# Kernel optimization log

Hardware: AMD Instinct MI355X
Metric: run time of the kernel (lower is better)

## Reference

```python
import jax, jax.numpy as jnp
import numpy as np

B = 65536
DIM = 8
HIS_LEN = 5
KIND_LEN = 10
HIS_ITEM_DIM = (1 + KIND_LEN) * DIM  # 88
ALL_DIM = DIM * (5 + KIND_LEN) + HIS_ITEM_DIM  # 208


def _linear_params(key, in_dim, out_dim):
    k1, k2 = jax.random.split(key)
    bound = 1.0 / np.sqrt(in_dim)
    w = jax.random.uniform(k1, (out_dim, in_dim), jnp.float32, -bound, bound)
    b = jax.random.uniform(k2, (out_dim,), jnp.float32, -bound, bound)
    return w, b


def setup_inputs() -> dict:
    key = jax.random.key(0)
    ks = jax.random.split(key, 20)
    inp = {
        'userid': jax.random.randint(ks[0], (B, 1), 0, 1000000),
        'itemid': jax.random.randint(ks[1], (B, 1), 0, 1000000),
        'user_age': jax.random.randint(ks[2], (B, 1), 0, 8),
        'gender': jax.random.randint(ks[3], (B, 1), 0, 3),
        'user_occupation': jax.random.randint(ks[4], (B, 1), 0, 25),
        'item_kind': jax.random.randint(ks[5], (B, KIND_LEN), 0, 20),
        'item_id_his': jax.random.randint(ks[6], (B, HIS_LEN), 0, 1000000),
        'item_kind_his': jax.random.randint(ks[7], (B, HIS_LEN, KIND_LEN), 0, 20),
        'user_emb': jax.random.normal(ks[8], (1000000, DIM), jnp.float32),
        'item_emb': jax.random.normal(ks[9], (1000000, DIM), jnp.float32),
        'age_emb': jax.random.normal(ks[10], (8, DIM), jnp.float32),
        'gender_emb': jax.random.normal(ks[11], (3, DIM), jnp.float32),
        'occ_emb': jax.random.normal(ks[12], (25, DIM), jnp.float32),
        'kind_emb': jax.random.normal(ks[13], (20, DIM), jnp.float32),
    }
    act_dims = [(HIS_ITEM_DIM * 3, 64), (64, 32), (32, 1)]
    for i, (di, do) in enumerate(act_dims, 1):
        w, b = _linear_params(jax.random.fold_in(key, 100 + i), di, do)
        inp[f'act_w{i}'], inp[f'act_b{i}'] = w, b
    mlp_dims = [(ALL_DIM, 128), (128, 64), (64, 32), (32, 1)]
    for i, (di, do) in enumerate(mlp_dims, 1):
        w, b = _linear_params(jax.random.fold_in(key, 200 + i), di, do)
        inp[f'mlp_w{i}'], inp[f'mlp_b{i}'] = w, b
    return inp


def _forward(userid, itemid, user_age, gender, user_occupation, item_kind,
             item_id_his, item_kind_his, user_emb, item_emb, age_emb,
             gender_emb, occ_emb, kind_emb,
             act_w1, act_b1, act_w2, act_b2, act_w3, act_b3,
             mlp_w1, mlp_b1, mlp_w2, mlp_b2, mlp_w3, mlp_b3, mlp_w4, mlp_b4):
    b = userid.shape[0]
    user_w = user_emb[userid]          # [b,1,8]
    item_w = item_emb[itemid]          # [b,1,8]
    age_w = age_emb[user_age]          # [b,1,8]
    gen_w = gender_emb[gender]         # [b,1,8]
    occ_w = occ_emb[user_occupation]   # [b,1,8]
    kind_w = kind_emb[item_kind]       # [b,10,8]
    kind_w = kind_w * (item_kind != 0)[..., None].astype(kind_w.dtype)

    # history: vectorized over his_len
    his_item_w = item_emb[item_id_his]           # [b,5,8]
    his_kind_w = kind_emb[item_kind_his]         # [b,5,10,8]
    his_kind_w = his_kind_w * (item_kind_his != 0)[..., None].astype(his_kind_w.dtype)
    his_feature = jnp.concatenate([his_item_w[:, :, None, :], his_kind_w], axis=2)
    his_feature = his_feature.reshape(b, HIS_LEN, HIS_ITEM_DIM)  # [b,5,88]

    item_feat_now = jnp.concatenate([item_w, kind_w], axis=1).reshape(b, 1, HIS_ITEM_DIM)
    item_feat_now = jnp.broadcast_to(item_feat_now, (b, HIS_LEN, HIS_ITEM_DIM))

    # ActUnit: i_in = [i1, i1-i2, i2]; score = MLP(i_in); act_weight = i1 * score
    i1, i2 = his_feature, item_feat_now
    i_in = jnp.concatenate([i1, i1 - i2, i2], axis=-1)  # [b,5,264]
    h = jax.nn.relu(jnp.einsum('bsd,od->bso', i_in, act_w1) + act_b1)
    h = jax.nn.relu(jnp.einsum('bsd,od->bso', h, act_w2) + act_b2)
    score = jnp.einsum('bsd,od->bso', h, act_w3) + act_b3  # [b,5,1]
    act_weight = i1 * score
    his_pool = jnp.sum(his_feature * act_weight, axis=1)  # [b,88]

    all_feat = jnp.concatenate([user_w, item_w, age_w, gen_w, occ_w, kind_w], axis=1).reshape(b, -1)
    all_feat = jnp.concatenate([all_feat, his_pool], axis=-1)  # [b,208]

    h = jax.nn.relu(all_feat @ mlp_w1.T + mlp_b1)
    h = jax.nn.relu(h @ mlp_w2.T + mlp_b2)
    h = jax.nn.relu(h @ mlp_w3.T + mlp_b3)
    logit = h @ mlp_w4.T + mlp_b4  # [b,1]
    return jax.nn.sigmoid(logit)


def reference(userid, itemid, user_age, gender, user_occupation, item_kind,
              item_id_his, item_kind_his, user_emb, item_emb, age_emb,
              gender_emb, occ_emb, kind_emb,
              act_w1, act_b1, act_w2, act_b2, act_w3, act_b3,
              mlp_w1, mlp_b1, mlp_w2, mlp_b2, mlp_w3, mlp_b3, mlp_w4, mlp_b4):
    return _forward(userid, itemid, user_age, gender, user_occupation, item_kind,
                    item_id_his, item_kind_his, user_emb, item_emb, age_emb,
                    gender_emb, occ_emb, kind_emb,
                    act_w1, act_b1, act_w2, act_b2, act_w3, act_b3,
                    mlp_w1, mlp_b1, mlp_w2, mlp_b2, mlp_w3, mlp_b3, mlp_w4, mlp_b4)
```

## Files before the change

### kernel.cpp

```cpp
#include <hip/hip_runtime.h>
#include <cstdint>
#include <math.h>

#define BATCH    65536
#define HIS_LEN  5
#define KIND_LEN 10
#define SB       64
#define NTH      256

typedef float    v2f __attribute__((ext_vector_type(2)));
typedef float    v4f __attribute__((ext_vector_type(4)));
typedef _Float16 v2h __attribute__((ext_vector_type(2)));
typedef _Float16 v8h __attribute__((ext_vector_type(8)));
__device__ __forceinline__ v2f mk2(float a, float b){ v2f r; r.x=a; r.y=b; return r; }
#define C2H(u)  __builtin_bit_cast(v2h,(unsigned)(u))
#define C8H(u4) __builtin_bit_cast(v8h,(u4))

#if __has_builtin(__builtin_amdgcn_fdot2)
__device__ __forceinline__ float FD2(v2h a, v2h b, float c){
  return __builtin_amdgcn_fdot2(a, b, c, false);
}
#else
__device__ __forceinline__ float FD2(v2h a, v2h b, float c){
  return c + (float)a.x*(float)b.x + (float)a.y*(float)b.y;
}
#endif

__device__ __forceinline__ unsigned short f2h(float f){
  return __builtin_bit_cast(unsigned short, (_Float16)f);
}
__device__ __forceinline__ unsigned pack2h(float a, float b){
  return (unsigned)f2h(a) | ((unsigned)f2h(b) << 16);
}
__device__ __forceinline__ v2h pkh(float a, float b){
  return __builtin_bit_cast(v2h, __builtin_amdgcn_cvt_pkrtz(a, b));
}

__device__ __forceinline__ void wlf(){
  asm volatile("s_waitcnt lgkmcnt(0)" ::: "memory");
  __builtin_amdgcn_sched_barrier(0);
}

#define OFF_HW1F 0
#define OFF_AW2F 6144
#define OFF_PF   7168
#define OFF_M3H  7428
#define OFF_MW1F 8452
#define OFF_MB1  22788
#define OFF_MW2F 22916
#define PREP_N   27012
#define AW2F4 1536
#define M3H4  1857
#define MW1F4 2113
#define MW2F4 5729

#define X2B   0
#define X1B   832
#define H1B   1664
#define H2B   2240
#define M3HL  2816
#define LAB1  12312
#define LAB2  12376
#define LW3   12408
#define LAB3  12440
#define LMB2  12441
#define LMB3  12505
#define LM4   12537
#define LMB4  12569
#define MB1F  12572
#define LDSF  12700

typedef const float* fp;

__device__ __forceinline__ float m1s_val(fp m1, int o, int q, int t){
  if(t >= 52) return 0.f;
  int src;
  if(t<8){ int E = (q==0)?0:(8+8*q); src = E + t; }
  else if(t<30){ int d=t-8; int idx = 8*(d>>1)+2*q+(d&1);
                 src = (idx<8) ? (8+idx) : (32+idx); }
  else { int d=t-30; int idx = 8*(d>>1)+2*q+(d&1); src = 120+idx; }
  return m1[o*208 + src];
}
__device__ __forceinline__ float m1k(fp m1, int o, int k){
  return m1s_val(m1, o, k/56, k%56);
}
__device__ __forceinline__ float w1c_val(fp aw1, int o, int q, int h, int d){
  if(d >= 22) return 0.f;
  int idx = 8*(d>>1) + 2*q + (d&1);
  return h ? (aw1[o*264+176+idx] - aw1[o*264+88+idx])
           : (aw1[o*264+idx]     + aw1[o*264+88+idx]);
}
__device__ __forceinline__ float hw1v(fp aw1, int o, int k){
  int h = (k >= 96) ? 1 : 0;
  int kk = k - 96*h;
  int q = kk/24, d = kk%24;
  return (d<22) ? w1c_val(aw1,o,q,h,d) : 0.f;
}

__global__ void din_prep(fp aw1, fp ab1, fp aw2, fp ab2, fp aw3, fp ab3,
                         fp m1,  fp mb1, fp m2,  fp mb2, fp m3,  fp mb3,
                         fp m4,  fp mb4, float* __restrict__ ws){
  int j = blockIdx.x*blockDim.x + threadIdx.x;
  unsigned* wsu = (unsigned*)ws;
  if(j < 6144){
    int frag = j>>2, jr = j&3;
    int lane = frag & 63, nt = frag >> 6;
    int n = nt/6, t = nt%6;
    int o = 16*n + (lane&15);
    int k0 = t*32 + ((lane>>4)<<3) + 2*jr;
    wsu[OFF_HW1F + j] = pack2h(hw1v(aw1,o,k0), hw1v(aw1,o,k0+1));
    return;
  } j -= 6144;
  if(j < 1024){
    int frag = j>>2, jr = j&3;
    int lane = frag & 63, nt = frag >> 6;
    int n2 = nt>>1, t2 = nt&1;
    int o = 16*n2 + (lane&15);
    int k0 = t2*32 + ((lane>>4)<<3) + 2*jr;
    wsu[OFF_AW2F + j] = pack2h(aw2[o*64 + k0], aw2[o*64 + k0+1]);
    return;
  } j -= 1024;
  if(j < 258){
    float v;
    if(j < 64)       v = ab1[j];
    else if(j < 96)  v = ab2[j-64];
    else if(j < 128) v = aw3[j-96];
    else if(j < 129) v = ab3[0];
    else if(j < 193) v = mb2[j-129];
    else if(j < 225) v = mb3[j-193];
    else if(j < 257) v = m4[j-225];
    else             v = mb4[0];
    ws[OFF_PF + j] = v; return;
  } j -= 258;
  if(j < 2){ ws[OFF_PF+258+j] = 0.f; return; } j -= 2;
  if(j < 1024){
    int qq = j>>8, rr = j&255, ip = rr>>5, dw = rr&31;
    wsu[OFF_M3H + j] = pack2h(m3[dw*64 + 16*qq + 2*ip], m3[dw*64 + 16*qq + 2*ip+1]);
    return;
  } j -= 1024;
  if(j < 14336){
    int frag = j>>2, jr = j&3;
    int lane = frag & 63, nt = frag >> 6;
    int n = nt/7, t = nt - 7*n;
    int o = 16*n + (lane&15);
    int k0 = t*32 + ((lane>>4)<<3) + 2*jr;
    wsu[OFF_MW1F + j] = pack2h(m1k(m1,o,k0), m1k(m1,o,k0+1));
    return;
  } j -= 14336;
  if(j < 128){ ws[OFF_MB1 + j] = mb1[j]; return; } j -= 128;
  if(j < 4096){
    int frag = j>>2, jr = j&3;
    int lane = frag & 63, nt = frag >> 6;
    int n2 = nt>>2, t2 = nt&3;
    int o = 16*n2 + (lane&15);
    int k0 = t2*32 + ((lane>>4)<<3) + 2*jr;
    wsu[OFF_MW2F + j] = pack2h(m2[o*128 + k0], m2[o*128 + k0+1]);
    return;
  }
}

template<int CTL>
__device__ __forceinline__ float qp(float v){
  return __uint_as_float((unsigned)__builtin_amdgcn_update_dpp(
      0, (int)__float_as_uint(v), CTL, 0xF, 0xF, true));
}
__device__ __forceinline__ float bsum4(float v){
  v += qp<0xB1>(v);
  v += qp<0x4E>(v);
  return v;
}

__device__ __forceinline__ void ldst16(void* l, const void* g){
  __builtin_amdgcn_global_load_lds(
      (const __attribute__((address_space(1))) unsigned int*)(uintptr_t)g,
      (__attribute__((address_space(3))) unsigned int*)(uintptr_t)l, 16, 0, 0);
}
__device__ __forceinline__ void ldst4(void* l, const void* g){
  __builtin_amdgcn_global_load_lds(
      (const __attribute__((address_space(1))) unsigned int*)(uintptr_t)g,
      (__attribute__((address_space(3))) unsigned int*)(uintptr_t)l, 4, 0, 0);
}

__device__ __forceinline__ void gather_h(const float2* __restrict__ itemp,
                                         const float2* __restrict__ kindp,
                                         int item_idx, const int* __restrict__ kidx,
                                         int q, v2h* f){
  float2 v = itemp[item_idx*4 + q];
  f[0] = pkh(v.x, v.y);
  #pragma unroll
  for(int r=0;r<KIND_LEN;r++){
    int ki = kidx[r];
    float2 w = kindp[ki*4 + q];
    float mx = ki ? w.x : 0.f, my = ki ? w.y : 0.f;
    f[1+r] = pkh(mx, my);
  }
}

__device__ __forceinline__ void write_X(float4* ls4, int base, int wid, int q,
                                        const v2h* f){
  unsigned xd[12];
  #pragma unroll
  for(int r=0;r<11;r++) xd[r] = __builtin_bit_cast(unsigned, f[r]);
  xd[11] = 0;
  uint4* xp = (uint4*)(ls4 + base + wid*13 + 3*q);
  #pragma unroll
  for(int c=0;c<3;c++){
    uint4 t; t.x=xd[4*c]; t.y=xd[4*c+1]; t.z=xd[4*c+2]; t.w=xd[4*c+3];
    xp[c] = t;
  }
}

__global__ void __launch_bounds__(NTH, 3)
din_main(const int* __restrict__ userid, const int* __restrict__ itemid,
         const int* __restrict__ age,    const int* __restrict__ gen,
         const int* __restrict__ occ,    const int* __restrict__ item_kind,
         const int* __restrict__ his_id, const int* __restrict__ his_kind,
         const float2* __restrict__ user_emb, const float2* __restrict__ item_emb,
         const float2* __restrict__ age_emb,  const float2* __restrict__ gen_emb,
         const float2* __restrict__ occ_emb,  const float2* __restrict__ kind_emb,
         const float* __restrict__ ws, float* __restrict__ out){
  const int tid  = threadIdx.x;
  const int q    = tid & 3;
  const int sl   = (tid & 63) >> 2;
  const int wv   = __builtin_amdgcn_readfirstlane(tid >> 6);
  const int wid  = wv*16 + sl;
  const int b    = blockIdx.x*SB + wid;
  const int l    = tid & 63;
  const int sr   = wv*16 + (l&15);
  const int kb   = l >> 4;

  __shared__ __align__(16) float ls[LDSF];
  float4* ls4 = (float4*)ls;
  const uint4* lsu4 = (const uint4*)ls;
  const float* wsc = ws;
  const float4* ws4 = (const float4*)ws;
  const uint4* wsu4 = (const uint4*)ws;

  ldst4(ls + LAB1 + tid, wsc + OFF_PF + tid);
  if(tid < 2)   ldst4(ls + LAB1 + 256 + tid, wsc + OFF_PF + 256 + tid);
  if(tid < 128) ldst4(ls + MB1F + tid, wsc + OFF_MB1 + tid);
  ldst16(ls4 + M3HL + (tid>>6)*66 + (tid&63), ws4 + M3H4 + tid);

  {
    v2h i2t[11];
    gather_h(item_emb, kind_emb, itemid[b], item_kind + b*KIND_LEN, q, i2t);
    write_X(ls4, X2B, wid, q, i2t);
  }
  v2h i1c[11], i1n[11];
  gather_h(item_emb, kind_emb, his_id[b*HIS_LEN], his_kind + b*HIS_LEN*KIND_LEN,
           q, i1c);

  v2f poolv[11];
  #pragma unroll
  for(int d=0;d<11;d++) poolv[d]=mk2(0.f,0.f);
  v2h i2h[11];
  float2 exr[4];

  __syncthreads();

  float hb1[4], hb2[2], w3r[8];
  #pragma unroll
  for(int n=0;n<4;n++)  hb1[n] = ls[LAB1 + 16*n + (l&15)];
  #pragma unroll
  for(int n2=0;n2<2;n2++) hb2[n2] = ls[LAB2 + 16*n2 + (l&15)];
  #pragma unroll
  for(int k=0;k<8;k++)  w3r[k] = ls[LW3 + 8*q + k];
  const float ab3v = ls[LAB3];
  uint4 awf[4];
  #pragma unroll
  for(int t=0;t<4;t++) awf[t] = wsu4[AW2F4 + t*64 + l];

  #pragma unroll 1
  for(int s=0;s<5;s++){
    wlf();
    write_X(ls4, X1B, wid, q, i1c);
    if(s < 4){
      gather_h(item_emb, kind_emb, his_id[b*HIS_LEN+s+1],
               his_kind + (b*HIS_LEN+s+1)*KIND_LEN, q, i1n);
    } else {
      gather_h(item_emb, kind_emb, itemid[b], item_kind + b*KIND_LEN, q, i2h);
      const float2* ep = (q==0)? user_emb : (q==1)? age_emb : (q==2)? gen_emb : occ_emb;
      int ei = (q==0)? userid[b] : (q==1)? age[b] : (q==2)? gen[b] : occ[b];
      #pragma unroll
      for(int k=0;k<4;k++) exr[k] = ep[ei*4+k];
    }
    wlf();
    {
      uint4 a1[6];
      #pragma unroll
      for(int t=0;t<3;t++) a1[t]   = lsu4[X1B + sr*13 + 4*t + kb];
      #pragma unroll
      for(int t=0;t<3;t++) a1[3+t] = lsu4[X2B + sr*13 + 4*t + kb];
      _Float16* h1p = (_Float16*)(ls4 + H1B);
      #pragma unroll
      for(int n=0;n<4;n++){
        float bb = hb1[n];
        v4f c = {bb,bb,bb,bb};
        #pragma unroll
        for(int t=0;t<6;t++){
          uint4 bw = wsu4[(n*6+t)*64 + l];
          c = __builtin_amdgcn_mfma_f32_16x16x32_f16(C8H(a1[t]), C8H(bw), c, 0, 0, 0);
        }
        #pragma unroll
        for(int i=0;i<4;i++)
          h1p[(16*wv + 4*kb + i)*72 + 16*n + (l&15)] = (_Float16)fmaxf(c[i],0.f);
      }
    }
    wlf();
    {
      uint4 a2[2];
      #pragma unroll
      for(int t=0;t<2;t++) a2[t] = lsu4[H1B + sr*9 + 4*t + kb];
      float* h2p = (float*)(ls4 + H2B);
      #pragma unroll
      for(int n2=0;n2<2;n2++){
        float bb = hb2[n2];
        v4f c = {bb,bb,bb,bb};
        #pragma unroll
        for(int t=0;t<2;t++){
          uint4 bw = awf[n2*2+t];
          c = __builtin_amdgcn_mfma_f32_16x16x32_f16(C8H(a2[t]), C8H(bw), c, 0, 0, 0);
        }
        #pragma unroll
        for(int i=0;i<4;i++)
          h2p[(16*wv + 4*kb + i)*36 + 16*n2 + (l&15)] = fmaxf(c[i],0.f);
      }
    }
    wlf();
    {
      const float4* hr = (const float4*)(ls4 + H2B + wid*9 + 2*q);
      float4 h0 = hr[0], h1v = hr[1];
      float scp = h0.x*w3r[0] + h0.y*w3r[1] + h0.z*w3r[2] + h0.w*w3r[3]
                + h1v.x*w3r[4] + h1v.y*w3r[5] + h1v.z*w3r[6] + h1v.w*w3r[7];
      float sc = bsum4(scp) + ab3v;
      #pragma unroll
      for(int j=0;j<11;j++){
        float sx = (float)i1c[j].x, sy = (float)i1c[j].y;
        poolv[j] = __builtin_elementwise_fma(mk2(sx*sc, sy*sc), mk2(sx, sy), poolv[j]);
      }
    }
    #pragma unroll
    for(int j=0;j<11;j++) i1c[j] = i1n[j];
  }

  v2h fe[26];
  #pragma unroll
  for(int k=0;k<4;k++) fe[k] = pkh(exr[k].x, exr[k].y);
  #pragma unroll
  for(int j=0;j<11;j++) fe[4+j]  = i2h[j];
  #pragma unroll
  for(int j=0;j<11;j++) fe[15+j] = pkh(poolv[j].x, poolv[j].y);

  __syncthreads();

  {
    unsigned xd[28];
    #pragma unroll
    for(int u=0;u<26;u++) xd[u] = __builtin_bit_cast(unsigned, fe[u]);
    xd[26] = 0; xd[27] = 0;
    uint4* xp = (uint4*)(ls4 + wid*29 + q*7);
    #pragma unroll
    for(int ct=0; ct<7; ct++){
      uint4 t; t.x=xd[4*ct]; t.y=xd[4*ct+1]; t.z=xd[4*ct+2]; t.w=xd[4*ct+3];
      xp[ct] = t;
    }
  }
  wlf();
  uint4 af[7];
  #pragma unroll
  for(int t=0;t<7;t++) af[t] = lsu4[sr*29 + t*4 + kb];
  __syncthreads();

  v4f acc1[8];
  #pragma unroll
  for(int n=0;n<8;n++){
    float bb = ls[MB1F + n*16 + (l&15)];
    v4f c = {bb, bb, bb, bb};
    #pragma unroll
    for(int t=0;t<7;t++){
      uint4 bw = wsu4[MW1F4 + (n*7+t)*64 + l];
      c = __builtin_amdgcn_mfma_f32_16x16x32_f16(C8H(af[t]), C8H(bw), c, 0, 0, 0);
    }
    acc1[n] = c;
  }
  {
    _Float16* h1p = (_Float16*)ls;
    #pragma unroll
    for(int n=0;n<8;n++)
      #pragma unroll
      for(int i=0;i<4;i++)
        h1p[(16*wv + 4*kb + i)*136 + 16*n + (l&15)] =
            (_Float16)fmaxf(acc1[n][i], 0.f);
  }
  wlf();

  v4f acc2[4];
  #pragma unroll
  for(int n2=0;n2<4;n2++){
    float bb = ls[LMB2 + n2*16 + (l&15)];
    v4f c = {bb, bb, bb, bb};
    acc2[n2] = c;
  }
  #pragma unroll
  for(int t2=0;t2<4;t2++){
    uint4 aw = lsu4[sr*17 + t2*4 + kb];
    #pragma unroll
    for(int n2=0;n2<4;n2++){
      uint4 bw = wsu4[MW2F4 + (n2*4+t2)*64 + l];
      acc2[n2] = __builtin_amdgcn_mfma_f32_16x16x32_f16(C8H(aw), C8H(bw), acc2[n2], 0, 0, 0);
    }
  }
  {
    _Float16* h2p = (_Float16*)(ls4 + 1088);
    #pragma unroll
    for(int n2=0;n2<4;n2++)
      #pragma unroll
      for(int i=0;i<4;i++)
        h2p[(16*wv + 4*kb + i)*72 + 16*n2 + (l&15)] =
            (_Float16)fmaxf(acc2[n2][i], 0.f);
  }
  wlf();

  v2h hp3[8];
  {
    const uint4* hr = (const uint4*)(ls4 + 1088 + wid*9 + 2*q);
    uint4 d0 = hr[0], d1 = hr[1];
    hp3[0]=C2H(d0.x); hp3[1]=C2H(d0.y); hp3[2]=C2H(d0.z); hp3[3]=C2H(d0.w);
    hp3[4]=C2H(d1.x); hp3[5]=C2H(d1.y); hp3[6]=C2H(d1.z); hp3[7]=C2H(d1.w);
  }
  float x = ls[LMB4];
  #pragma unroll
  for(int g=0;g<4;g++){
    float a[8];
    #pragma unroll
    for(int j=0;j<8;j++) a[j]=0.f;
    #pragma unroll
    for(int ip=0;ip<8;ip++){
      const uint4* w3p = (const uint4*)(ls4 + M3HL + q*66 + ip*8 + 2*g);
      uint4 b0=w3p[0], b1=w3p[1];
      a[0]=FD2(C2H(b0.x),hp3[ip],a[0]); a[1]=FD2(C2H(b0.y),hp3[ip],a[1]);
      a[2]=FD2(C2H(b0.z),hp3[ip],a[2]); a[3]=FD2(C2H(b0.w),hp3[ip],a[3]);
      a[4]=FD2(C2H(b1.x),hp3[ip],a[4]); a[5]=FD2(C2H(b1.y),hp3[ip],a[5]);
      a[6]=FD2(C2H(b1.z),hp3[ip],a[6]); a[7]=FD2(C2H(b1.w),hp3[ip],a[7]);
    }
    #pragma unroll
    for(int j=0;j<8;j++) a[j] = bsum4(a[j]);
    #pragma unroll
    for(int j=0;j<8;j++)
      x += ls[LM4+8*g+j] * fmaxf(a[j] + ls[LMB3+8*g+j], 0.f);
  }

  if(q==0) out[b] = 1.0f/(1.0f + __expf(-x));
}

extern "C" void kernel_launch(void* const* d_in, const int* in_sizes, int n_in,
                              void* d_out, int out_size, void* d_ws, size_t ws_size,
                              hipStream_t stream){
  const int* userid    = (const int*)d_in[0];
  const int* itemid    = (const int*)d_in[1];
  const int* age       = (const int*)d_in[2];
  const int* gen       = (const int*)d_in[3];
  const int* occ       = (const int*)d_in[4];
  const int* item_kind = (const int*)d_in[5];
  const int* his_id    = (const int*)d_in[6];
  const int* his_kind  = (const int*)d_in[7];
  const float2* user_emb = (const float2*)d_in[8];
  const float2* item_emb = (const float2*)d_in[9];
  const float2* age_emb  = (const float2*)d_in[10];
  const float2* gen_emb  = (const float2*)d_in[11];
  const float2* occ_emb  = (const float2*)d_in[12];
  const float2* kind_emb = (const float2*)d_in[13];
  float* ws = (float*)d_ws;

  din_prep<<<(PREP_N+255)/256, 256, 0, stream>>>(
      (fp)d_in[14], (fp)d_in[15], (fp)d_in[16], (fp)d_in[17], (fp)d_in[18], (fp)d_in[19],
      (fp)d_in[20], (fp)d_in[21], (fp)d_in[22], (fp)d_in[23], (fp)d_in[24], (fp)d_in[25],
      (fp)d_in[26], (fp)d_in[27], ws);

  din_main<<<BATCH/SB, NTH, 0, stream>>>(
      userid, itemid, age, gen, occ, item_kind, his_id, his_kind,
      user_emb, item_emb, age_emb, gen_emb, occ_emb, kind_emb,
      ws, (float*)d_out);
}
```

Before: 284.9 us.

## Prefetch all history gathers upfront and use block barriers instead of wave waits

Issues all five history-item gathers, the target item gather and the extra embedding lookups before the attention loop, replacing the one-step-ahead prefetch. The loop is fully unrolled over register-held history. The per-wave lgkmcnt waits are replaced with block-wide __syncthreads, and the attention layer-2 weights are reloaded from global memory each step instead of being kept in registers. This exposes more memory-level parallelism for the random gathers, but raises register pressure (55 extra half2 registers) and adds block-level synchronisation that may cut occupancy and overlap.

```diff
diff --git a/kernel.cpp b/kernel.cpp
--- a/kernel.cpp
+++ b/kernel.cpp
@@ -34,11 +34,6 @@
 }
 __device__ __forceinline__ v2h pkh(float a, float b){
   return __builtin_bit_cast(v2h, __builtin_amdgcn_cvt_pkrtz(a, b));
-}
-
-__device__ __forceinline__ void wlf(){
-  asm volatile("s_waitcnt lgkmcnt(0)" ::: "memory");
-  __builtin_amdgcn_sched_barrier(0);
 }
 
 #define OFF_HW1F 0
@@ -241,20 +236,27 @@
   if(tid < 128) ldst4(ls + MB1F + tid, wsc + OFF_MB1 + tid);
   ldst16(ls4 + M3HL + (tid>>6)*66 + (tid&63), ws4 + M3H4 + tid);
 
+  v2h i2h[11];
+  gather_h(item_emb, kind_emb, itemid[b], item_kind + b*KIND_LEN, q, i2h);
+  write_X(ls4, X2B, wid, q, i2h);
+
+  v2h i1a[5][11];
+  #pragma unroll
+  for(int s=0;s<5;s++)
+    gather_h(item_emb, kind_emb, his_id[b*HIS_LEN+s],
+             his_kind + (b*HIS_LEN+s)*KIND_LEN, q, i1a[s]);
+
+  v2h feex[4];
   {
-    v2h i2t[11];
-    gather_h(item_emb, kind_emb, itemid[b], item_kind + b*KIND_LEN, q, i2t);
-    write_X(ls4, X2B, wid, q, i2t);
-  }
-  v2h i1c[11], i1n[11];
-  gather_h(item_emb, kind_emb, his_id[b*HIS_LEN], his_kind + b*HIS_LEN*KIND_LEN,
-           q, i1c);
+    const float2* ep = (q==0)? user_emb : (q==1)? age_emb : (q==2)? gen_emb : occ_emb;
+    int ei = (q==0)? userid[b] : (q==1)? age[b] : (q==2)? gen[b] : occ[b];
+    #pragma unroll
+    for(int k=0;k<4;k++){ float2 v = ep[ei*4+k]; feex[k] = pkh(v.x, v.y); }
+  }
 
   v2f poolv[11];
   #pragma unroll
   for(int d=0;d<11;d++) poolv[d]=mk2(0.f,0.f);
-  v2h i2h[11];
-  float2 exr[4];
 
   __syncthreads();
 
@@ -266,25 +268,11 @@
   #pragma unroll
   for(int k=0;k<8;k++)  w3r[k] = ls[LW3 + 8*q + k];
   const float ab3v = ls[LAB3];
-  uint4 awf[4];
-  #pragma unroll
-  for(int t=0;t<4;t++) awf[t] = wsu4[AW2F4 + t*64 + l];
-
-  #pragma unroll 1
+
+  #pragma unroll
   for(int s=0;s<5;s++){
-    wlf();
-    write_X(ls4, X1B, wid, q, i1c);
-    if(s < 4){
-      gather_h(item_emb, kind_emb, his_id[b*HIS_LEN+s+1],
-               his_kind + (b*HIS_LEN+s+1)*KIND_LEN, q, i1n);
-    } else {
-      gather_h(item_emb, kind_emb, itemid[b], item_kind + b*KIND_LEN, q, i2h);
-      const float2* ep = (q==0)? user_emb : (q==1)? age_emb : (q==2)? gen_emb : occ_emb;
-      int ei = (q==0)? userid[b] : (q==1)? age[b] : (q==2)? gen[b] : occ[b];
-      #pragma unroll
-      for(int k=0;k<4;k++) exr[k] = ep[ei*4+k];
-    }
-    wlf();
+    write_X(ls4, X1B, wid, q, i1a[s]);
+    __syncthreads();
     {
       uint4 a1[6];
       #pragma unroll
@@ -306,7 +294,7 @@
           h1p[(16*wv + 4*kb + i)*72 + 16*n + (l&15)] = (_Float16)fmaxf(c[i],0.f);
       }
     }
-    wlf();
+    __syncthreads();
     {
       uint4 a2[2];
       #pragma unroll
@@ -318,7 +306,7 @@
         v4f c = {bb,bb,bb,bb};
         #pragma unroll
         for(int t=0;t<2;t++){
-          uint4 bw = awf[n2*2+t];
+          uint4 bw = wsu4[AW2F4 + (n2*2+t)*64 + l];
           c = __builtin_amdgcn_mfma_f32_16x16x32_f16(C8H(a2[t]), C8H(bw), c, 0, 0, 0);
         }
         #pragma unroll
@@ -326,7 +314,7 @@
           h2p[(16*wv + 4*kb + i)*36 + 16*n2 + (l&15)] = fmaxf(c[i],0.f);
       }
     }
-    wlf();
+    __syncthreads();
     {
       const float4* hr = (const float4*)(ls4 + H2B + wid*9 + 2*q);
       float4 h0 = hr[0], h1v = hr[1];
@@ -335,17 +323,15 @@
       float sc = bsum4(scp) + ab3v;
       #pragma unroll
       for(int j=0;j<11;j++){
-        float sx = (float)i1c[j].x, sy = (float)i1c[j].y;
+        float sx = (float)i1a[s][j].x, sy = (float)i1a[s][j].y;
         poolv[j] = __builtin_elementwise_fma(mk2(sx*sc, sy*sc), mk2(sx, sy), poolv[j]);
       }
     }
-    #pragma unroll
-    for(int j=0;j<11;j++) i1c[j] = i1n[j];
   }
 
   v2h fe[26];
   #pragma unroll
-  for(int k=0;k<4;k++) fe[k] = pkh(exr[k].x, exr[k].y);
+  for(int k=0;k<4;k++) fe[k] = feex[k];
   #pragma unroll
   for(int j=0;j<11;j++) fe[4+j]  = i2h[j];
   #pragma unroll
@@ -365,7 +351,7 @@
       xp[ct] = t;
     }
   }
-  wlf();
+  __syncthreads();
   uint4 af[7];
   #pragma unroll
   for(int t=0;t<7;t++) af[t] = lsu4[sr*29 + t*4 + kb];
@@ -392,7 +378,7 @@
         h1p[(16*wv + 4*kb + i)*136 + 16*n + (l&15)] =
             (_Float16)fmaxf(acc1[n][i], 0.f);
   }
-  wlf();
+  __syncthreads();
 
   v4f acc2[4];
   #pragma unroll
@@ -419,7 +405,7 @@
         h2p[(16*wv + 4*kb + i)*72 + 16*n2 + (l&15)] =
             (_Float16)fmaxf(acc2[n2][i], 0.f);
   }
-  wlf();
+  __syncthreads();
 
   v2h hp3[8];
   {
```

Result: faster. 251.8 us (-11.6%).
